# Kernel tuning notes

Measured on AMD Instinct MI355X. Metric: run time of the kernel, lower is better.

Reference implementation:

```python
import jax, jax.numpy as jnp
import numpy as np

N_NODES = 100000
N_EDGES = 1600000
NIN = 128
NOUT = 128


def setup_inputs() -> dict:
    key = jax.random.key(0)
    k1, k2, k3, k4, k5 = jax.random.split(key, 5)
    x = jax.random.normal(k1, (N_NODES, NIN), dtype=jnp.float32)
    edge_index = jax.random.randint(k2, (2, N_EDGES), 0, N_NODES, dtype=jnp.int32)
    edge_attr = jax.random.uniform(k3, (N_EDGES,), dtype=jnp.float32)
    # GCNConv linear weight (glorot-ish scale) and bias
    W = jax.random.normal(k4, (NIN, NOUT), dtype=jnp.float32) / np.sqrt(NIN)
    b = jnp.zeros((NOUT,), dtype=jnp.float32)
    return {"x": x, "edge_index": edge_index, "edge_attr": edge_attr, "W": W, "b": b}


def reference(x, edge_index, edge_attr, W, b):
    # PyG GCNConv: out = D^{-1/2} (A + I) D^{-1/2} X W + b
    # edge_attr is accepted by the wrapper's forward but ignored.
    N = x.shape[0]
    src, dst = edge_index[0], edge_index[1]
    # add self-loops
    loops = jnp.arange(N, dtype=edge_index.dtype)
    src = jnp.concatenate([src, loops])
    dst = jnp.concatenate([dst, loops])
    # degree over destination nodes (unit edge weights + self loops)
    deg = jax.ops.segment_sum(jnp.ones_like(dst, dtype=x.dtype), dst, num_segments=N)
    dinv = jnp.where(deg > 0, jax.lax.rsqrt(deg), 0.0)
    norm = dinv[src] * dinv[dst]  # [E + N]
    h = x @ W  # [N, NOUT] — project before aggregation (PyG order)
    msgs = h[src] * norm[:, None]  # [E + N, NOUT] gathered messages
    out = jax.ops.segment_sum(msgs, dst, num_segments=N) + b
    return out
```

## Files before the change

### kernel.cpp

```cpp
#include <hip/hip_runtime.h>
#include <hip/hip_bf16.h>


#define NIN 128
#define NOUT 128
#define NPART 8
#define G_GROUPS 98
#define MAXD 64
#define WPITCH 68

typedef __attribute__((ext_vector_type(8))) short short8;
typedef __attribute__((ext_vector_type(4))) float f32x4;
typedef __attribute__((ext_vector_type(4))) int   i32x4;
typedef __attribute__((ext_vector_type(4))) float f32x4v;

__device__ __forceinline__ float bf2f(unsigned short u) {
    unsigned v = ((unsigned)u) << 16;
    return __uint_as_float(v);
}
__device__ __forceinline__ unsigned short f2bf(float f) {
    unsigned u = __float_as_uint(f);
    unsigned r = 0x7FFFu + ((u >> 16) & 1u);
    return (unsigned short)((u + r) >> 16);
}

__global__ __launch_bounds__(256, 8) void k_build(const float* __restrict__ x,
                                                  const float* __restrict__ W,
                                                  const int* __restrict__ ei,
                                                  int* __restrict__ cnt,
                                                  int* __restrict__ adj,
                                                  unsigned short* __restrict__ h,
                                                  int E, int N, int gb) {
    __shared__ unsigned short Wt[128 * WPITCH];

    int grp = blockIdx.x >> 5;
    int s   = blockIdx.x & 31;

    if ((s & 15) >= 8) {
        int p = s & 7;
        int o = (s >> 4) & 1;
        int c = grp * 2 + o;
        int PS = (N + NPART - 1) / NPART;
        int lo = p * PS, hi = min(N, lo + PS);
        int nchunk = 2 * G_GROUPS;
        int chunkE = (((E + nchunk - 1) / nchunk) + 3) & ~3;
        int e0 = c * chunkE, e1 = min(E, e0 + chunkE);
        for (int e = e0 + (int)threadIdx.x * 4; e < e1; e += 1024) {
            i32x4 s4 = *(const i32x4*)(ei + e);
            i32x4 d4 = *(const i32x4*)(ei + E + e);
            #pragma unroll
            for (int k = 0; k < 4; k++) {
                int d = d4[k];
                if (d >= lo && d < hi) {
                    int pos = atomicAdd(&cnt[d], 1);
                    if (pos < MAXD) adj[(size_t)d * MAXD + pos] = s4[k];
                }
            }
        }
        return;
    }

    int rid = grp * 16 + (s & 7) + ((s >> 4) & 1) * 8;
    if (rid >= gb) return;

    int wave = threadIdx.x >> 6, lane = threadIdx.x & 63;
    int node_base = rid * 64 + wave * 16;
    bool active = node_base < N;
    int c = lane & 15, quad = lane >> 4;

    const f32x4v* xrow = (const f32x4v*)(x + (size_t)(node_base + c) * NIN + quad * 8);

    f32x4 acc[8];
    #pragma unroll
    for (int nt = 0; nt < 8; nt++) acc[nt] = (f32x4)(0.0f);

    for (int idx = threadIdx.x; idx < 64 * 128; idx += 256) {
        int kk = idx >> 7, n = idx & 127;
        Wt[n * WPITCH + kk] = f2bf(W[kk * 128 + n]);
    }
    __syncthreads();

    if (active) {
        short8 a0, a1;
        {
            f32x4v f0 = __builtin_nontemporal_load(xrow + 0);
            f32x4v f1 = __builtin_nontemporal_load(xrow + 1);
            f32x4v g0 = __builtin_nontemporal_load(xrow + 8);
            f32x4v g1 = __builtin_nontemporal_load(xrow + 9);
            a0[0]=(short)f2bf(f0[0]); a0[1]=(short)f2bf(f0[1]); a0[2]=(short)f2bf(f0[2]); a0[3]=(short)f2bf(f0[3]);
            a0[4]=(short)f2bf(f1[0]); a0[5]=(short)f2bf(f1[1]); a0[6]=(short)f2bf(f1[2]); a0[7]=(short)f2bf(f1[3]);
            a1[0]=(short)f2bf(g0[0]); a1[1]=(short)f2bf(g0[1]); a1[2]=(short)f2bf(g0[2]); a1[3]=(short)f2bf(g0[3]);
            a1[4]=(short)f2bf(g1[0]); a1[5]=(short)f2bf(g1[1]); a1[6]=(short)f2bf(g1[2]); a1[7]=(short)f2bf(g1[3]);
        }
        #pragma unroll
        for (int nt = 0; nt < 8; nt++) {
            const unsigned short* wp = &Wt[(nt * 16 + c) * WPITCH + quad * 8];
            short8 b0 = *(const short8*)(wp);
            short8 b1 = *(const short8*)(wp + 32);
            acc[nt] = __builtin_amdgcn_mfma_f32_16x16x32_bf16(a0, b0, acc[nt], 0, 0, 0);
            acc[nt] = __builtin_amdgcn_mfma_f32_16x16x32_bf16(a1, b1, acc[nt], 0, 0, 0);
        }
    }
    __syncthreads();

    for (int idx = threadIdx.x; idx < 64 * 128; idx += 256) {
        int kk = idx >> 7, n = idx & 127;
        Wt[n * WPITCH + kk] = f2bf(W[(kk + 64) * 128 + n]);
    }
    __syncthreads();

    if (active) {
        short8 a2, a3;
        {
            f32x4v f0 = __builtin_nontemporal_load(xrow + 16);
            f32x4v f1 = __builtin_nontemporal_load(xrow + 17);
            f32x4v g0 = __builtin_nontemporal_load(xrow + 24);
            f32x4v g1 = __builtin_nontemporal_load(xrow + 25);
            a2[0]=(short)f2bf(f0[0]); a2[1]=(short)f2bf(f0[1]); a2[2]=(short)f2bf(f0[2]); a2[3]=(short)f2bf(f0[3]);
            a2[4]=(short)f2bf(f1[0]); a2[5]=(short)f2bf(f1[1]); a2[6]=(short)f2bf(f1[2]); a2[7]=(short)f2bf(f1[3]);
            a3[0]=(short)f2bf(g0[0]); a3[1]=(short)f2bf(g0[1]); a3[2]=(short)f2bf(g0[2]); a3[3]=(short)f2bf(g0[3]);
            a3[4]=(short)f2bf(g1[0]); a3[5]=(short)f2bf(g1[1]); a3[6]=(short)f2bf(g1[2]); a3[7]=(short)f2bf(g1[3]);
        }
        #pragma unroll
        for (int nt = 0; nt < 8; nt++) {
            const unsigned short* wp = &Wt[(nt * 16 + c) * WPITCH + quad * 8];
            short8 b0 = *(const short8*)(wp);
            short8 b1 = *(const short8*)(wp + 32);
            acc[nt] = __builtin_amdgcn_mfma_f32_16x16x32_bf16(a2, b0, acc[nt], 0, 0, 0);
            acc[nt] = __builtin_amdgcn_mfma_f32_16x16x32_bf16(a3, b1, acc[nt], 0, 0, 0);
        }

        #pragma unroll
        for (int nt = 0; nt < 8; nt++) {
            #pragma unroll
            for (int r = 0; r < 4; r++) {
                int node = node_base + quad * 4 + r;
                h[(size_t)node * NOUT + nt * 16 + c] = f2bf(acc[nt][r]);
            }
        }
    }
}

__global__ __launch_bounds__(256) void k_scale(unsigned short* __restrict__ h,
                                               const int* __restrict__ cnt, int N) {
    int idx = blockIdx.x * 256 + threadIdx.x;
    int total = N * (NOUT / 8);
    if (idx >= total) return;
    int node = idx >> 4;
    float dv = rsqrtf((float)(cnt[node] + 1));
    uint4* hq = (uint4*)h;
    uint4 v = hq[idx];
    unsigned r[4] = { v.x, v.y, v.z, v.w };
    #pragma unroll
    for (int w = 0; w < 4; w++) {
        float lo = bf2f((unsigned short)(r[w] & 0xFFFF)) * dv;
        float hi = bf2f((unsigned short)(r[w] >> 16)) * dv;
        r[w] = (unsigned)f2bf(lo) | ((unsigned)f2bf(hi) << 16);
    }
    v.x = r[0]; v.y = r[1]; v.z = r[2]; v.w = r[3];
    hq[idx] = v;
}

__global__ __launch_bounds__(256) void k_agg(const unsigned short* __restrict__ h,
                                             const int* __restrict__ cnt,
                                             const int* __restrict__ adj,
                                             const float* __restrict__ bias,
                                             float* __restrict__ out, int N) {
    int wave = threadIdx.x >> 6, lane = threadIdx.x & 63;
    int half = lane >> 5, sub = lane & 31;
    int node = blockIdx.x * 4 + wave;
    if (node >= N) return;

    int degc = cnt[node];
    float dn = rsqrtf((float)(degc + 1));
    int e0 = node * MAXD;
    int e1 = e0 + min(degc, MAXD);

    const uint2* hp = (const uint2*)h;
    float a0 = 0.f, a1 = 0.f, a2 = 0.f, a3 = 0.f;

    {
        int s = half ? ((e0 < e1) ? adj[e0] : node) : node;
        uint2 v = hp[(size_t)s * 32 + sub];
        if (!half || (e0 < e1)) {
            a0 += bf2f((unsigned short)(v.x & 0xFFFF));
            a1 += bf2f((unsigned short)(v.x >> 16));
            a2 += bf2f((unsigned short)(v.y & 0xFFFF));
            a3 += bf2f((unsigned short)(v.y >> 16));
        }
    }

    int e = e0 + 1;
    for (; e + 7 < e1; e += 8) {
        #pragma unroll
        for (int k = 0; k < 4; k++) {
            int s = adj[e + 2 * k + half];
            uint2 v = hp[(size_t)s * 32 + sub];
            a0 += bf2f((unsigned short)(v.x & 0xFFFF));
            a1 += bf2f((unsigned short)(v.x >> 16));
            a2 += bf2f((unsigned short)(v.y & 0xFFFF));
            a3 += bf2f((unsigned short)(v.y >> 16));
        }
    }
    for (; e + 1 < e1; e += 2) {
        int s = adj[e + half];
        uint2 v = hp[(size_t)s * 32 + sub];
        a0 += bf2f((unsigned short)(v.x & 0xFFFF));
        a1 += bf2f((unsigned short)(v.x >> 16));
        a2 += bf2f((unsigned short)(v.y & 0xFFFF));
        a3 += bf2f((unsigned short)(v.y >> 16));
    }
    if (e < e1) {
        int s = adj[e];
        uint2 v = hp[(size_t)s * 32 + sub];
        if (!half) {
            a0 += bf2f((unsigned short)(v.x & 0xFFFF));
            a1 += bf2f((unsigned short)(v.x >> 16));
            a2 += bf2f((unsigned short)(v.y & 0xFFFF));
            a3 += bf2f((unsigned short)(v.y >> 16));
        }
    }

    a0 += __shfl_xor(a0, 32);
    a1 += __shfl_xor(a1, 32);
    a2 += __shfl_xor(a2, 32);
    a3 += __shfl_xor(a3, 32);

    if (!half) {
        float4 b4 = ((const float4*)bias)[sub];
        f32x4 o;
        o[0] = a0 * dn + b4.x;
        o[1] = a1 * dn + b4.y;
        o[2] = a2 * dn + b4.z;
        o[3] = a3 * dn + b4.w;
        __builtin_nontemporal_store(o, (f32x4*)(out + (size_t)node * NOUT) + sub);
    }
}

static inline size_t align256(size_t v) { return (v + 255) & ~(size_t)255; }

extern "C" void kernel_launch(void* const* d_in, const int* in_sizes, int n_in,
                              void* d_out, int out_size, void* d_ws, size_t ws_size,
                              hipStream_t stream) {
    const float* x  = (const float*)d_in[0];
    const int*   ei = (const int*)d_in[1];
    const float* W  = (const float*)d_in[3];
    const float* b  = (const float*)d_in[4];
    float*       out = (float*)d_out;

    int N = in_sizes[0] / NIN;
    int E = in_sizes[1] / 2;
    int gb = (N + 63) / 64;

    char* ws = (char*)d_ws;
    size_t o = 0;
    int*   cnt = (int*)(ws + o);   o += align256((size_t)N * 4);
    int*   adj = (int*)(ws + o);   o += align256((size_t)N * MAXD * 4);
    unsigned short* h = (unsigned short*)(ws + o); o += align256((size_t)N * NOUT * 2);
    (void)ws_size; (void)n_in; (void)out_size;

    hipMemsetAsync(cnt, 0, (size_t)N * 4, stream);
    k_build<<<32 * G_GROUPS, 256, 0, stream>>>(x, W, ei, cnt, adj, h, E, N, gb);
    k_scale<<<(N * (NOUT / 8) + 255) / 256, 256, 0, stream>>>(h, cnt, N);
    k_agg<<<(N + 3) / 4, 256, 0, stream>>>(h, cnt, adj, b, out, N);
}
```

Before: 271.4 us.

## Fuse build, scale and aggregate into one persistent cooperative kernel with grid syncs

Replaces the memset and three kernel launches with a single cooperative persistent kernel. Grid-wide syncs separate four phases: zeroing counts, the projection GEMM overlapped with adjacency build, degree scaling, and aggregation. Each phase uses grid-stride loops over a grid capped at 2048 blocks, and the edge loop prefetches the next edge chunk. This removes launch gaps and kernel tails, but adds grid-sync cost and forces one register/occupancy budget across all phases, which may hurt the gather-heavy aggregation phase.

```diff
diff --git a/kernel.cpp b/kernel.cpp
--- a/kernel.cpp
+++ b/kernel.cpp
@@ -1,11 +1,13 @@
 #include <hip/hip_runtime.h>
 #include <hip/hip_bf16.h>
+#include <hip/hip_cooperative_groups.h>
+
+namespace cg = cooperative_groups;
 
 
 #define NIN 128
 #define NOUT 128
 #define NPART 8
-#define G_GROUPS 98
 #define MAXD 64
 #define WPITCH 68
 
@@ -24,216 +26,228 @@
     return (unsigned short)((u + r) >> 16);
 }
 
-__global__ __launch_bounds__(256, 8) void k_build(const float* __restrict__ x,
-                                                  const float* __restrict__ W,
-                                                  const int* __restrict__ ei,
-                                                  int* __restrict__ cnt,
-                                                  int* __restrict__ adj,
-                                                  unsigned short* __restrict__ h,
-                                                  int E, int N, int gb) {
+__global__ __launch_bounds__(256, 8) void k_all(const float* __restrict__ x,
+                                                const float* __restrict__ W,
+                                                const int* __restrict__ ei,
+                                                int* __restrict__ cnt,
+                                                int* __restrict__ adj,
+                                                unsigned short* __restrict__ h,
+                                                const float* __restrict__ bias,
+                                                float* __restrict__ out,
+                                                int E, int N, int gb) {
+    cg::grid_group gridg = cg::this_grid();
     __shared__ unsigned short Wt[128 * WPITCH];
 
-    int grp = blockIdx.x >> 5;
-    int s   = blockIdx.x & 31;
-
-    if ((s & 15) >= 8) {
-        int p = s & 7;
-        int o = (s >> 4) & 1;
-        int c = grp * 2 + o;
-        int PS = (N + NPART - 1) / NPART;
-        int lo = p * PS, hi = min(N, lo + PS);
-        int nchunk = 2 * G_GROUPS;
-        int chunkE = (((E + nchunk - 1) / nchunk) + 3) & ~3;
-        int e0 = c * chunkE, e1 = min(E, e0 + chunkE);
-        for (int e = e0 + (int)threadIdx.x * 4; e < e1; e += 1024) {
-            i32x4 s4 = *(const i32x4*)(ei + e);
-            i32x4 d4 = *(const i32x4*)(ei + E + e);
+    const int nb  = gridDim.x;
+    const int bid = blockIdx.x;
+    const int tid = threadIdx.x;
+
+    for (int i = bid * 256 + tid; i < N; i += nb * 256) cnt[i] = 0;
+    __threadfence();
+    gridg.sync();
+
+    {
+        int grp = bid >> 5, slot = bid & 31, ngrp = nb >> 5;
+        if (slot < 8) {
+            int wave = tid >> 6, lane = tid & 63;
+            int c = lane & 15, quad = lane >> 4;
+            for (int t = grp * 8 + slot; t < gb; t += ngrp * 8) {
+                int node_base = t * 64 + wave * 16;
+                bool active = node_base < N;
+                const f32x4v* xrow =
+                    (const f32x4v*)(x + (size_t)(node_base + c) * NIN + quad * 8);
+
+                f32x4 acc[8];
+                #pragma unroll
+                for (int nt = 0; nt < 8; nt++) acc[nt] = (f32x4)(0.0f);
+
+                __syncthreads();
+                for (int idx = tid; idx < 64 * 128; idx += 256) {
+                    int kk = idx >> 7, n = idx & 127;
+                    Wt[n * WPITCH + kk] = f2bf(W[kk * 128 + n]);
+                }
+                __syncthreads();
+                if (active) {
+                    short8 a0, a1;
+                    f32x4v f0 = __builtin_nontemporal_load(xrow + 0);
+                    f32x4v f1 = __builtin_nontemporal_load(xrow + 1);
+                    f32x4v g0 = __builtin_nontemporal_load(xrow + 8);
+                    f32x4v g1 = __builtin_nontemporal_load(xrow + 9);
+                    a0[0]=(short)f2bf(f0[0]); a0[1]=(short)f2bf(f0[1]); a0[2]=(short)f2bf(f0[2]); a0[3]=(short)f2bf(f0[3]);
+                    a0[4]=(short)f2bf(f1[0]); a0[5]=(short)f2bf(f1[1]); a0[6]=(short)f2bf(f1[2]); a0[7]=(short)f2bf(f1[3]);
+                    a1[0]=(short)f2bf(g0[0]); a1[1]=(short)f2bf(g0[1]); a1[2]=(short)f2bf(g0[2]); a1[3]=(short)f2bf(g0[3]);
+                    a1[4]=(short)f2bf(g1[0]); a1[5]=(short)f2bf(g1[1]); a1[6]=(short)f2bf(g1[2]); a1[7]=(short)f2bf(g1[3]);
+                    #pragma unroll
+                    for (int nt = 0; nt < 8; nt++) {
+                        const unsigned short* wp = &Wt[(nt * 16 + c) * WPITCH + quad * 8];
+                        short8 b0 = *(const short8*)(wp);
+                        short8 b1 = *(const short8*)(wp + 32);
+                        acc[nt] = __builtin_amdgcn_mfma_f32_16x16x32_bf16(a0, b0, acc[nt], 0, 0, 0);
+                        acc[nt] = __builtin_amdgcn_mfma_f32_16x16x32_bf16(a1, b1, acc[nt], 0, 0, 0);
+                    }
+                }
+                __syncthreads();
+                for (int idx = tid; idx < 64 * 128; idx += 256) {
+                    int kk = idx >> 7, n = idx & 127;
+                    Wt[n * WPITCH + kk] = f2bf(W[(kk + 64) * 128 + n]);
+                }
+                __syncthreads();
+                if (active) {
+                    short8 a2, a3;
+                    f32x4v f0 = __builtin_nontemporal_load(xrow + 16);
+                    f32x4v f1 = __builtin_nontemporal_load(xrow + 17);
+                    f32x4v g0 = __builtin_nontemporal_load(xrow + 24);
+                    f32x4v g1 = __builtin_nontemporal_load(xrow + 25);
+                    a2[0]=(short)f2bf(f0[0]); a2[1]=(short)f2bf(f0[1]); a2[2]=(short)f2bf(f0[2]); a2[3]=(short)f2bf(f0[3]);
+                    a2[4]=(short)f2bf(f1[0]); a2[5]=(short)f2bf(f1[1]); a2[6]=(short)f2bf(f1[2]); a2[7]=(short)f2bf(f1[3]);
+                    a3[0]=(short)f2bf(g0[0]); a3[1]=(short)f2bf(g0[1]); a3[2]=(short)f2bf(g0[2]); a3[3]=(short)f2bf(g0[3]);
+                    a3[4]=(short)f2bf(g1[0]); a3[5]=(short)f2bf(g1[1]); a3[6]=(short)f2bf(g1[2]); a3[7]=(short)f2bf(g1[3]);
+                    #pragma unroll
+                    for (int nt = 0; nt < 8; nt++) {
+                        const unsigned short* wp = &Wt[(nt * 16 + c) * WPITCH + quad * 8];
+                        short8 b0 = *(const short8*)(wp);
+                        short8 b1 = *(const short8*)(wp + 32);
+                        acc[nt] = __builtin_amdgcn_mfma_f32_16x16x32_bf16(a2, b0, acc[nt], 0, 0, 0);
+                        acc[nt] = __builtin_amdgcn_mfma_f32_16x16x32_bf16(a3, b1, acc[nt], 0, 0, 0);
+                    }
+                    #pragma unroll
+                    for (int nt = 0; nt < 8; nt++) {
+                        #pragma unroll
+                        for (int r = 0; r < 4; r++) {
+                            int node = node_base + quad * 4 + r;
+                            h[(size_t)node * NOUT + nt * 16 + c] = f2bf(acc[nt][r]);
+                        }
+                    }
+                }
+            }
+        } else {
+            int p = slot & 7, j = (slot - 8) >> 3;
+            int PS = (N + NPART - 1) / NPART;
+            int lo = p * PS, hi = min(N, lo + PS);
+            int nchunk = 3 * ngrp;
+            int chunkE = (((E + nchunk - 1) / nchunk) + 3) & ~3;
+            int cch = grp * 3 + j;
+            int e0 = cch * chunkE, e1 = min(E, e0 + chunkE);
+
+            auto proc = [&](i32x4 s4, i32x4 d4) {
+                #pragma unroll
+                for (int k = 0; k < 4; k++) {
+                    int d = d4[k];
+                    if (d >= lo && d < hi) {
+                        int pos = atomicAdd(&cnt[d], 1);
+                        if (pos < MAXD) adj[(size_t)d * MAXD + pos] = s4[k];
+                    }
+                }
+            };
+
+            int e = e0 + tid * 4;
+            if (e < e1) {
+                i32x4 s4 = *(const i32x4*)(ei + e);
+                i32x4 d4 = *(const i32x4*)(ei + E + e);
+                for (int en = e + 1024; en < e1; en += 1024) {
+                    i32x4 s4n = *(const i32x4*)(ei + en);
+                    i32x4 d4n = *(const i32x4*)(ei + E + en);
+                    proc(s4, d4);
+                    s4 = s4n; d4 = d4n;
+                }
+                proc(s4, d4);
+            }
+        }
+    }
+    __threadfence();
+    gridg.sync();
+
+    {
+        int total = N * (NOUT / 8);
+        uint4* hq = (uint4*)h;
+        for (int idx = bid * 256 + tid; idx < total; idx += nb * 256) {
+            int node = idx >> 4;
+            float dv = rsqrtf((float)(cnt[node] + 1));
+            uint4 v = hq[idx];
+            unsigned r[4] = { v.x, v.y, v.z, v.w };
             #pragma unroll
-            for (int k = 0; k < 4; k++) {
-                int d = d4[k];
-                if (d >= lo && d < hi) {
-                    int pos = atomicAdd(&cnt[d], 1);
-                    if (pos < MAXD) adj[(size_t)d * MAXD + pos] = s4[k];
-                }
-            }
+            for (int w = 0; w < 4; w++) {
+                float lo = bf2f((unsigned short)(r[w] & 0xFFFF)) * dv;
+                float hi = bf2f((unsigned short)(r[w] >> 16)) * dv;
+                r[w] = (unsigned)f2bf(lo) | ((unsigned)f2bf(hi) << 16);
+            }
+            v.x = r[0]; v.y = r[1]; v.z = r[2]; v.w = r[3];
+            hq[idx] = v;
         }
-        return;
-    }
-
-    int rid = grp * 16 + (s & 7) + ((s >> 4) & 1) * 8;
-    if (rid >= gb) return;
-
-    int wave = threadIdx.x >> 6, lane = threadIdx.x & 63;
-    int node_base = rid * 64 + wave * 16;
-    bool active = node_base < N;
-    int c = lane & 15, quad = lane >> 4;
-
-    const f32x4v* xrow = (const f32x4v*)(x + (size_t)(node_base + c) * NIN + quad * 8);
-
-    f32x4 acc[8];
-    #pragma unroll
-    for (int nt = 0; nt < 8; nt++) acc[nt] = (f32x4)(0.0f);
-
-    for (int idx = threadIdx.x; idx < 64 * 128; idx += 256) {
-        int kk = idx >> 7, n = idx & 127;
-        Wt[n * WPITCH + kk] = f2bf(W[kk * 128 + n]);
-    }
-    __syncthreads();
-
-    if (active) {
-        short8 a0, a1;
-        {
-            f32x4v f0 = __builtin_nontemporal_load(xrow + 0);
-            f32x4v f1 = __builtin_nontemporal_load(xrow + 1);
-            f32x4v g0 = __builtin_nontemporal_load(xrow + 8);
-            f32x4v g1 = __builtin_nontemporal_load(xrow + 9);
-            a0[0]=(short)f2bf(f0[0]); a0[1]=(short)f2bf(f0[1]); a0[2]=(short)f2bf(f0[2]); a0[3]=(short)f2bf(f0[3]);
-            a0[4]=(short)f2bf(f1[0]); a0[5]=(short)f2bf(f1[1]); a0[6]=(short)f2bf(f1[2]); a0[7]=(short)f2bf(f1[3]);
-            a1[0]=(short)f2bf(g0[0]); a1[1]=(short)f2bf(g0[1]); a1[2]=(short)f2bf(g0[2]); a1[3]=(short)f2bf(g0[3]);
-            a1[4]=(short)f2bf(g1[0]); a1[5]=(short)f2bf(g1[1]); a1[6]=(short)f2bf(g1[2]); a1[7]=(short)f2bf(g1[3]);
+    }
+    __threadfence();
+    gridg.sync();
+
+    {
+        int wave = tid >> 6, lane = tid & 63;
+        int half = lane >> 5, sub = lane & 31;
+        const uint2* hp = (const uint2*)h;
+
+        for (int node = bid * 4 + wave; node < N; node += nb * 4) {
+            int degc = cnt[node];
+            float dn = rsqrtf((float)(degc + 1));
+            int e0 = node * MAXD;
+            int e1 = e0 + min(degc, MAXD);
+
+            float a0 = 0.f, a1 = 0.f, a2 = 0.f, a3 = 0.f;
+
+            {
+                int s = half ? ((e0 < e1) ? adj[e0] : node) : node;
+                uint2 v = hp[(size_t)s * 32 + sub];
+                if (!half || (e0 < e1)) {
+                    a0 += bf2f((unsigned short)(v.x & 0xFFFF));
+                    a1 += bf2f((unsigned short)(v.x >> 16));
+                    a2 += bf2f((unsigned short)(v.y & 0xFFFF));
+                    a3 += bf2f((unsigned short)(v.y >> 16));
+                }
+            }
+
+            int e = e0 + 1;
+            for (; e + 7 < e1; e += 8) {
+                #pragma unroll
+                for (int k = 0; k < 4; k++) {
+                    int s = adj[e + 2 * k + half];
+                    uint2 v = hp[(size_t)s * 32 + sub];
+                    a0 += bf2f((unsigned short)(v.x & 0xFFFF));
+                    a1 += bf2f((unsigned short)(v.x >> 16));
+                    a2 += bf2f((unsigned short)(v.y & 0xFFFF));
+                    a3 += bf2f((unsigned short)(v.y >> 16));
+                }
+            }
+            for (; e + 1 < e1; e += 2) {
+                int s = adj[e + half];
+                uint2 v = hp[(size_t)s * 32 + sub];
+                a0 += bf2f((unsigned short)(v.x & 0xFFFF));
+                a1 += bf2f((unsigned short)(v.x >> 16));
+                a2 += bf2f((unsigned short)(v.y & 0xFFFF));
+                a3 += bf2f((unsigned short)(v.y >> 16));
+            }
+            if (e < e1) {
+                int s = adj[e];
+                uint2 v = hp[(size_t)s * 32 + sub];
+                if (!half) {
+                    a0 += bf2f((unsigned short)(v.x & 0xFFFF));
+                    a1 += bf2f((unsigned short)(v.x >> 16));
+                    a2 += bf2f((unsigned short)(v.y & 0xFFFF));
+                    a3 += bf2f((unsigned short)(v.y >> 16));
+                }
+            }
+
+            a0 += __shfl_xor(a0, 32);
+            a1 += __shfl_xor(a1, 32);
+            a2 += __shfl_xor(a2, 32);
+            a3 += __shfl_xor(a3, 32);
+
+            if (!half) {
+                float4 b4 = ((const float4*)bias)[sub];
+                f32x4 o;
+                o[0] = a0 * dn + b4.x;
+                o[1] = a1 * dn + b4.y;
+                o[2] = a2 * dn + b4.z;
+                o[3] = a3 * dn + b4.w;
+                __builtin_nontemporal_store(o, (f32x4*)(out + (size_t)node * NOUT) + sub);
+            }
         }
-        #pragma unroll
-        for (int nt = 0; nt < 8; nt++) {
-            const unsigned short* wp = &Wt[(nt * 16 + c) * WPITCH + quad * 8];
-            short8 b0 = *(const short8*)(wp);
-            short8 b1 = *(const short8*)(wp + 32);
-            acc[nt] = __builtin_amdgcn_mfma_f32_16x16x32_bf16(a0, b0, acc[nt], 0, 0, 0);
-            acc[nt] = __builtin_amdgcn_mfma_f32_16x16x32_bf16(a1, b1, acc[nt], 0, 0, 0);
-        }
-    }
-    __syncthreads();
-
-    for (int idx = threadIdx.x; idx < 64 * 128; idx += 256) {
-        int kk = idx >> 7, n = idx & 127;
-        Wt[n * WPITCH + kk] = f2bf(W[(kk + 64) * 128 + n]);
-    }
-    __syncthreads();
-
-    if (active) {
-        short8 a2, a3;
-        {
-            f32x4v f0 = __builtin_nontemporal_load(xrow + 16);
-            f32x4v f1 = __builtin_nontemporal_load(xrow + 17);
-            f32x4v g0 = __builtin_nontemporal_load(xrow + 24);
-            f32x4v g1 = __builtin_nontemporal_load(xrow + 25);
-            a2[0]=(short)f2bf(f0[0]); a2[1]=(short)f2bf(f0[1]); a2[2]=(short)f2bf(f0[2]); a2[3]=(short)f2bf(f0[3]);
-            a2[4]=(short)f2bf(f1[0]); a2[5]=(short)f2bf(f1[1]); a2[6]=(short)f2bf(f1[2]); a2[7]=(short)f2bf(f1[3]);
-            a3[0]=(short)f2bf(g0[0]); a3[1]=(short)f2bf(g0[1]); a3[2]=(short)f2bf(g0[2]); a3[3]=(short)f2bf(g0[3]);
-            a3[4]=(short)f2bf(g1[0]); a3[5]=(short)f2bf(g1[1]); a3[6]=(short)f2bf(g1[2]); a3[7]=(short)f2bf(g1[3]);
-        }
-        #pragma unroll
-        for (int nt = 0; nt < 8; nt++) {
-            const unsigned short* wp = &Wt[(nt * 16 + c) * WPITCH + quad * 8];
-            short8 b0 = *(const short8*)(wp);
-            short8 b1 = *(const short8*)(wp + 32);
-            acc[nt] = __builtin_amdgcn_mfma_f32_16x16x32_bf16(a2, b0, acc[nt], 0, 0, 0);
-            acc[nt] = __builtin_amdgcn_mfma_f32_16x16x32_bf16(a3, b1, acc[nt], 0, 0, 0);
-        }
-
-        #pragma unroll
-        for (int nt = 0; nt < 8; nt++) {
-            #pragma unroll
-            for (int r = 0; r < 4; r++) {
-                int node = node_base + quad * 4 + r;
-                h[(size_t)node * NOUT + nt * 16 + c] = f2bf(acc[nt][r]);
-            }
-        }
-    }
-}
-
-__global__ __launch_bounds__(256) void k_scale(unsigned short* __restrict__ h,
-                                               const int* __restrict__ cnt, int N) {
-    int idx = blockIdx.x * 256 + threadIdx.x;
-    int total = N * (NOUT / 8);
-    if (idx >= total) return;
-    int node = idx >> 4;
-    float dv = rsqrtf((float)(cnt[node] + 1));
-    uint4* hq = (uint4*)h;
-    uint4 v = hq[idx];
-    unsigned r[4] = { v.x, v.y, v.z, v.w };
-    #pragma unroll
-    for (int w = 0; w < 4; w++) {
-        float lo = bf2f((unsigned short)(r[w] & 0xFFFF)) * dv;
-        float hi = bf2f((unsigned short)(r[w] >> 16)) * dv;
-        r[w] = (unsigned)f2bf(lo) | ((unsigned)f2bf(hi) << 16);
-    }
-    v.x = r[0]; v.y = r[1]; v.z = r[2]; v.w = r[3];
-    hq[idx] = v;
-}
-
-__global__ __launch_bounds__(256) void k_agg(const unsigned short* __restrict__ h,
-                                             const int* __restrict__ cnt,
-                                             const int* __restrict__ adj,
-                                             const float* __restrict__ bias,
-                                             float* __restrict__ out, int N) {
-    int wave = threadIdx.x >> 6, lane = threadIdx.x & 63;
-    int half = lane >> 5, sub = lane & 31;
-    int node = blockIdx.x * 4 + wave;
-    if (node >= N) return;
-
-    int degc = cnt[node];
-    float dn = rsqrtf((float)(degc + 1));
-    int e0 = node * MAXD;
-    int e1 = e0 + min(degc, MAXD);
-
-    const uint2* hp = (const uint2*)h;
-    float a0 = 0.f, a1 = 0.f, a2 = 0.f, a3 = 0.f;
-
-    {
-        int s = half ? ((e0 < e1) ? adj[e0] : node) : node;
-        uint2 v = hp[(size_t)s * 32 + sub];
-        if (!half || (e0 < e1)) {
-            a0 += bf2f((unsigned short)(v.x & 0xFFFF));
-            a1 += bf2f((unsigned short)(v.x >> 16));
-            a2 += bf2f((unsigned short)(v.y & 0xFFFF));
-            a3 += bf2f((unsigned short)(v.y >> 16));
-        }
-    }
-
-    int e = e0 + 1;
-    for (; e + 7 < e1; e += 8) {
-        #pragma unroll
-        for (int k = 0; k < 4; k++) {
-            int s = adj[e + 2 * k + half];
-            uint2 v = hp[(size_t)s * 32 + sub];
-            a0 += bf2f((unsigned short)(v.x & 0xFFFF));
-            a1 += bf2f((unsigned short)(v.x >> 16));
-            a2 += bf2f((unsigned short)(v.y & 0xFFFF));
-            a3 += bf2f((unsigned short)(v.y >> 16));
-        }
-    }
-    for (; e + 1 < e1; e += 2) {
-        int s = adj[e + half];
-        uint2 v = hp[(size_t)s * 32 + sub];
-        a0 += bf2f((unsigned short)(v.x & 0xFFFF));
-        a1 += bf2f((unsigned short)(v.x >> 16));
-        a2 += bf2f((unsigned short)(v.y & 0xFFFF));
-        a3 += bf2f((unsigned short)(v.y >> 16));
-    }
-    if (e < e1) {
-        int s = adj[e];
-        uint2 v = hp[(size_t)s * 32 + sub];
-        if (!half) {
-            a0 += bf2f((unsigned short)(v.x & 0xFFFF));
-            a1 += bf2f((unsigned short)(v.x >> 16));
-            a2 += bf2f((unsigned short)(v.y & 0xFFFF));
-            a3 += bf2f((unsigned short)(v.y >> 16));
-        }
-    }
-
-    a0 += __shfl_xor(a0, 32);
-    a1 += __shfl_xor(a1, 32);
-    a2 += __shfl_xor(a2, 32);
-    a3 += __shfl_xor(a3, 32);
-
-    if (!half) {
-        float4 b4 = ((const float4*)bias)[sub];
-        f32x4 o;
-        o[0] = a0 * dn + b4.x;
-        o[1] = a1 * dn + b4.y;
-        o[2] = a2 * dn + b4.z;
-        o[3] = a3 * dn + b4.w;
-        __builtin_nontemporal_store(o, (f32x4*)(out + (size_t)node * NOUT) + sub);
     }
 }
 
@@ -259,8 +273,21 @@
     unsigned short* h = (unsigned short*)(ws + o); o += align256((size_t)N * NOUT * 2);
     (void)ws_size; (void)n_in; (void)out_size;
 
-    hipMemsetAsync(cnt, 0, (size_t)N * 4, stream);
-    k_build<<<32 * G_GROUPS, 256, 0, stream>>>(x, W, ei, cnt, adj, h, E, N, gb);
-    k_scale<<<(N * (NOUT / 8) + 255) / 256, 256, 0, stream>>>(h, cnt, N);
-    k_agg<<<(N + 3) / 4, 256, 0, stream>>>(h, cnt, adj, b, out, N);
-}
+    static int nb_blocks = 0;
+    if (nb_blocks == 0) {
+        int maxb = 0;
+        if (hipOccupancyMaxActiveBlocksPerMultiprocessor(&maxb, k_all, 256, 0)
+                != hipSuccess || maxb <= 0)
+            maxb = 4;
+        long nbl = (long)maxb * 256;
+        if (nbl > 2048) nbl = 2048;
+        nbl &= ~31L;
+        if (nbl < 32) nbl = 32;
+        nb_blocks = (int)nbl;
+    }
+
+    void* args[] = { (void*)&x, (void*)&W, (void*)&ei, (void*)&cnt, (void*)&adj,
+                     (void*)&h, (void*)&b, (void*)&out, (void*)&E, (void*)&N,
+                     (void*)&gb };
+    hipLaunchCooperativeKernel(k_all, dim3(nb_blocks), dim3(256), args, 0, stream);
+}
```

Result: slower. 916.2 us (+237.6%).

## Replace partitioned edge scatter with unpartitioned scatter and persistent GEMM block loop

Applied to the files above, without the earlier changes.

Edge-scatter blocks no longer split destinations into 8 node partitions that each re-read the full edge chunk. Each edge is now read once and inserted directly with an atomic. The GEMM part becomes a grid-stride loop over 64-node tiles, so a fixed grid of 2048 blocks (24 of every 32 slots doing GEMM, 8 scattering) covers all tiles. This removes redundant edge-list reads, but it drops whatever atomic locality the partitioning gave and reloads W into shared memory for every tile.

```diff
diff --git a/kernel.cpp b/kernel.cpp
--- a/kernel.cpp
+++ b/kernel.cpp
@@ -4,10 +4,9 @@
 
 #define NIN 128
 #define NOUT 128
-#define NPART 8
-#define G_GROUPS 98
 #define MAXD 64
 #define WPITCH 68
+#define NB_BUILD 2048
 
 typedef __attribute__((ext_vector_type(8))) short short8;
 typedef __attribute__((ext_vector_type(4))) float f32x4;
@@ -33,56 +32,49 @@
                                                   int E, int N, int gb) {
     __shared__ unsigned short Wt[128 * WPITCH];
 
-    int grp = blockIdx.x >> 5;
-    int s   = blockIdx.x & 31;
-
-    if ((s & 15) >= 8) {
-        int p = s & 7;
-        int o = (s >> 4) & 1;
-        int c = grp * 2 + o;
-        int PS = (N + NPART - 1) / NPART;
-        int lo = p * PS, hi = min(N, lo + PS);
-        int nchunk = 2 * G_GROUPS;
-        int chunkE = (((E + nchunk - 1) / nchunk) + 3) & ~3;
-        int e0 = c * chunkE, e1 = min(E, e0 + chunkE);
+    int grp  = blockIdx.x >> 5;
+    int slot = blockIdx.x & 31;
+    int ngrp = gridDim.x >> 5;
+
+    if (slot >= 24) {
+        int rid = grp * 8 + (slot - 24);
+        int nscat = ngrp * 8;
+        int chunkE = (((E + nscat - 1) / nscat) + 3) & ~3;
+        int e0 = rid * chunkE, e1 = min(E, e0 + chunkE);
         for (int e = e0 + (int)threadIdx.x * 4; e < e1; e += 1024) {
             i32x4 s4 = *(const i32x4*)(ei + e);
             i32x4 d4 = *(const i32x4*)(ei + E + e);
             #pragma unroll
             for (int k = 0; k < 4; k++) {
                 int d = d4[k];
-                if (d >= lo && d < hi) {
-                    int pos = atomicAdd(&cnt[d], 1);
-                    if (pos < MAXD) adj[(size_t)d * MAXD + pos] = s4[k];
-                }
+                int pos = atomicAdd(&cnt[d], 1);
+                if (pos < MAXD) adj[(size_t)d * MAXD + pos] = s4[k];
             }
         }
         return;
     }
 
-    int rid = grp * 16 + (s & 7) + ((s >> 4) & 1) * 8;
-    if (rid >= gb) return;
-
     int wave = threadIdx.x >> 6, lane = threadIdx.x & 63;
-    int node_base = rid * 64 + wave * 16;
-    bool active = node_base < N;
     int c = lane & 15, quad = lane >> 4;
 
-    const f32x4v* xrow = (const f32x4v*)(x + (size_t)(node_base + c) * NIN + quad * 8);
-
-    f32x4 acc[8];
-    #pragma unroll
-    for (int nt = 0; nt < 8; nt++) acc[nt] = (f32x4)(0.0f);
-
-    for (int idx = threadIdx.x; idx < 64 * 128; idx += 256) {
-        int kk = idx >> 7, n = idx & 127;
-        Wt[n * WPITCH + kk] = f2bf(W[kk * 128 + n]);
-    }
-    __syncthreads();
-
-    if (active) {
-        short8 a0, a1;
-        {
+    for (int t = grp * 24 + slot; t < gb; t += ngrp * 24) {
+        int node_base = t * 64 + wave * 16;
+        bool active = node_base < N;
+        const f32x4v* xrow = (const f32x4v*)(x + (size_t)(node_base + c) * NIN + quad * 8);
+
+        f32x4 acc[8];
+        #pragma unroll
+        for (int nt = 0; nt < 8; nt++) acc[nt] = (f32x4)(0.0f);
+
+        __syncthreads();
+        for (int idx = threadIdx.x; idx < 64 * 128; idx += 256) {
+            int kk = idx >> 7, n = idx & 127;
+            Wt[n * WPITCH + kk] = f2bf(W[kk * 128 + n]);
+        }
+        __syncthreads();
+
+        if (active) {
+            short8 a0, a1;
             f32x4v f0 = __builtin_nontemporal_load(xrow + 0);
             f32x4v f1 = __builtin_nontemporal_load(xrow + 1);
             f32x4v g0 = __builtin_nontemporal_load(xrow + 8);
@@ -91,27 +83,24 @@
             a0[4]=(short)f2bf(f1[0]); a0[5]=(short)f2bf(f1[1]); a0[6]=(short)f2bf(f1[2]); a0[7]=(short)f2bf(f1[3]);
             a1[0]=(short)f2bf(g0[0]); a1[1]=(short)f2bf(g0[1]); a1[2]=(short)f2bf(g0[2]); a1[3]=(short)f2bf(g0[3]);
             a1[4]=(short)f2bf(g1[0]); a1[5]=(short)f2bf(g1[1]); a1[6]=(short)f2bf(g1[2]); a1[7]=(short)f2bf(g1[3]);
-        }
-        #pragma unroll
-        for (int nt = 0; nt < 8; nt++) {
-            const unsigned short* wp = &Wt[(nt * 16 + c) * WPITCH + quad * 8];
-            short8 b0 = *(const short8*)(wp);
-            short8 b1 = *(const short8*)(wp + 32);
-            acc[nt] = __builtin_amdgcn_mfma_f32_16x16x32_bf16(a0, b0, acc[nt], 0, 0, 0);
-            acc[nt] = __builtin_amdgcn_mfma_f32_16x16x32_bf16(a1, b1, acc[nt], 0, 0, 0);
-        }
-    }
-    __syncthreads();
-
-    for (int idx = threadIdx.x; idx < 64 * 128; idx += 256) {
-        int kk = idx >> 7, n = idx & 127;
-        Wt[n * WPITCH + kk] = f2bf(W[(kk + 64) * 128 + n]);
-    }
-    __syncthreads();
-
-    if (active) {
-        short8 a2, a3;
-        {
+            #pragma unroll
+            for (int nt = 0; nt < 8; nt++) {
+                const unsigned short* wp = &Wt[(nt * 16 + c) * WPITCH + quad * 8];
+                short8 b0 = *(const short8*)(wp);
+                short8 b1 = *(const short8*)(wp + 32);
+                acc[nt] = __builtin_amdgcn_mfma_f32_16x16x32_bf16(a0, b0, acc[nt], 0, 0, 0);
+                acc[nt] = __builtin_amdgcn_mfma_f32_16x16x32_bf16(a1, b1, acc[nt], 0, 0, 0);
+            }
+        }
+        __syncthreads();
+        for (int idx = threadIdx.x; idx < 64 * 128; idx += 256) {
+            int kk = idx >> 7, n = idx & 127;
+            Wt[n * WPITCH + kk] = f2bf(W[(kk + 64) * 128 + n]);
+        }
+        __syncthreads();
+
+        if (active) {
+            short8 a2, a3;
             f32x4v f0 = __builtin_nontemporal_load(xrow + 16);
             f32x4v f1 = __builtin_nontemporal_load(xrow + 17);
             f32x4v g0 = __builtin_nontemporal_load(xrow + 24);
@@ -120,22 +109,22 @@
             a2[4]=(short)f2bf(f1[0]); a2[5]=(short)f2bf(f1[1]); a2[6]=(short)f2bf(f1[2]); a2[7]=(short)f2bf(f1[3]);
             a3[0]=(short)f2bf(g0[0]); a3[1]=(short)f2bf(g0[1]); a3[2]=(short)f2bf(g0[2]); a3[3]=(short)f2bf(g0[3]);
             a3[4]=(short)f2bf(g1[0]); a3[5]=(short)f2bf(g1[1]); a3[6]=(short)f2bf(g1[2]); a3[7]=(short)f2bf(g1[3]);
-        }
-        #pragma unroll
-        for (int nt = 0; nt < 8; nt++) {
-            const unsigned short* wp = &Wt[(nt * 16 + c) * WPITCH + quad * 8];
-            short8 b0 = *(const short8*)(wp);
-            short8 b1 = *(const short8*)(wp + 32);
-            acc[nt] = __builtin_amdgcn_mfma_f32_16x16x32_bf16(a2, b0, acc[nt], 0, 0, 0);
-            acc[nt] = __builtin_amdgcn_mfma_f32_16x16x32_bf16(a3, b1, acc[nt], 0, 0, 0);
-        }
-
-        #pragma unroll
-        for (int nt = 0; nt < 8; nt++) {
-            #pragma unroll
-            for (int r = 0; r < 4; r++) {
-                int node = node_base + quad * 4 + r;
-                h[(size_t)node * NOUT + nt * 16 + c] = f2bf(acc[nt][r]);
+            #pragma unroll
+            for (int nt = 0; nt < 8; nt++) {
+                const unsigned short* wp = &Wt[(nt * 16 + c) * WPITCH + quad * 8];
+                short8 b0 = *(const short8*)(wp);
+                short8 b1 = *(const short8*)(wp + 32);
+                acc[nt] = __builtin_amdgcn_mfma_f32_16x16x32_bf16(a2, b0, acc[nt], 0, 0, 0);
+                acc[nt] = __builtin_amdgcn_mfma_f32_16x16x32_bf16(a3, b1, acc[nt], 0, 0, 0);
+            }
+
+            #pragma unroll
+            for (int nt = 0; nt < 8; nt++) {
+                #pragma unroll
+                for (int r = 0; r < 4; r++) {
+                    int node = node_base + quad * 4 + r;
+                    h[(size_t)node * NOUT + nt * 16 + c] = f2bf(acc[nt][r]);
+                }
             }
         }
     }
@@ -260,7 +249,7 @@
     (void)ws_size; (void)n_in; (void)out_size;
 
     hipMemsetAsync(cnt, 0, (size_t)N * 4, stream);
-    k_build<<<32 * G_GROUPS, 256, 0, stream>>>(x, W, ei, cnt, adj, h, E, N, gb);
+    k_build<<<NB_BUILD, 256, 0, stream>>>(x, W, ei, cnt, adj, h, E, N, gb);
     k_scale<<<(N * (NOUT / 8) + 255) / 256, 256, 0, stream>>>(h, cnt, N);
     k_agg<<<(N + 3) / 4, 256, 0, stream>>>(h, cnt, adj, b, out, N);
 }
```

Measured after the change: 296.5 us. 1.09x slower.
